# Performance work log

Measured on AMD Instinct MI355X. Metric: run time of the kernel, lower is better.

Reference implementation:

```python
import math
import jax, jax.numpy as jnp
import numpy as np


def get_alibi_slopes(n_heads: int) -> jnp.ndarray:
    def _pow2_slopes(n):
        i = jnp.arange(1, n + 1, dtype=jnp.float32)
        return jnp.power(2.0, -8.0 * i / n)
    if n_heads & (n_heads - 1) == 0:
        return _pow2_slopes(n_heads)
    nearest = 2 ** math.ceil(math.log2(n_heads))
    full = _pow2_slopes(nearest)
    half = nearest // 2
    half_slopes = _pow2_slopes(half)
    extra = full[jnp.arange(half) * 2 + 1]
    return jnp.concatenate([half_slopes, extra])[:n_heads]


def build_alibi_bias(n_heads: int, T: int, causal: bool = True) -> jnp.ndarray:
    slopes = get_alibi_slopes(n_heads)  # (H,)
    idx = jnp.arange(T)
    rel = jnp.abs(idx[:, None] - idx[None, :]).astype(jnp.float32)  # (T,T)
    bias = -slopes[:, None, None] * rel[None]  # (H,T,T)
    if causal:
        future = idx[None, :] > idx[:, None]
        bias = jnp.where(future[None], -jnp.inf, bias)
    return bias


def setup_inputs() -> dict:
    key = jax.random.key(0)
    ks = jax.random.split(key, 5)
    B, T, C = 2, 2048, 1024
    s = 0.02
    return {
        "x": jax.random.normal(ks[0], (B, T, C), dtype=jnp.float32),
        "Wq": jax.random.normal(ks[1], (C, C), dtype=jnp.float32) * s,
        "Wk": jax.random.normal(ks[2], (C, C), dtype=jnp.float32) * s,
        "Wv": jax.random.normal(ks[3], (C, C), dtype=jnp.float32) * s,
        "Wo": jax.random.normal(ks[4], (C, C), dtype=jnp.float32) * s,
    }


def reference(x, Wq, Wk, Wv, Wo):
    B, T, C = x.shape
    H = 16
    D = C // H
    scale = D ** -0.5
    # torch nn.Linear(bias=False): y = x @ W.T
    def proj_split(W):
        t = jnp.einsum('btc,dc->btd', x, W)
        return t.reshape(B, T, H, D).transpose(0, 2, 1, 3)  # (B,H,T,D)
    q, k, v = proj_split(Wq), proj_split(Wk), proj_split(Wv)
    scores = jnp.einsum('bhtd,bhsd->bhts', q, k) * scale  # (B,H,T,T)
    bias = build_alibi_bias(H, T, causal=True)  # (H,T,T)
    scores = scores + bias[None]
    attn = jax.nn.softmax(scores, axis=-1)
    out = jnp.einsum('bhts,bhsd->bhtd', attn, v)
    out = out.transpose(0, 2, 1, 3).reshape(B, T, C)
    return jnp.einsum('btc,dc->btd', out, Wo)
```

## Files before the change

### kernel.cpp

```cpp
#include <hip/hip_runtime.h>
#include <hip/hip_bf16.h>


typedef _Float16 f16;
typedef f16 f16x2 __attribute__((ext_vector_type(2)));
typedef f16 f16x4 __attribute__((ext_vector_type(4)));
typedef f16 f16x8 __attribute__((ext_vector_type(8)));
typedef float f32x4 __attribute__((ext_vector_type(4)));
typedef float f32x16 __attribute__((ext_vector_type(16)));

#define LOG2E 1.4426950408889634f
#define LDA 72
#define LDV 136

typedef const __attribute__((address_space(1))) unsigned int* gas1;
typedef __attribute__((address_space(3))) unsigned int* las3;
__device__ __forceinline__ void gload16(const f16* g, f16* l) {
  __builtin_amdgcn_global_load_lds((gas1)g, (las3)l, 16, 0, 0);
}

__device__ __forceinline__ f16x4 pk4(f32x4 v) {
  f16x2 a = __builtin_bit_cast(f16x2, __builtin_amdgcn_cvt_pkrtz(v[0], v[1]));
  f16x2 b = __builtin_bit_cast(f16x2, __builtin_amdgcn_cvt_pkrtz(v[2], v[3]));
  f16x4 r; r[0] = a[0]; r[1] = a[1]; r[2] = b[0]; r[3] = b[1];
  return r;
}
__device__ __forceinline__ f16x8 mkp(const float* e, int p) {
  f16x2 a = __builtin_bit_cast(f16x2, __builtin_amdgcn_cvt_pkrtz(e[4*p+0], e[4*p+1]));
  f16x2 b = __builtin_bit_cast(f16x2, __builtin_amdgcn_cvt_pkrtz(e[4*p+2], e[4*p+3]));
  f16x2 c = __builtin_bit_cast(f16x2, __builtin_amdgcn_cvt_pkrtz(e[8+4*p+0], e[8+4*p+1]));
  f16x2 d = __builtin_bit_cast(f16x2, __builtin_amdgcn_cvt_pkrtz(e[8+4*p+2], e[8+4*p+3]));
  f16x8 r;
  r[0]=a[0]; r[1]=a[1]; r[2]=b[0]; r[3]=b[1];
  r[4]=c[0]; r[5]=c[1]; r[6]=d[0]; r[7]=d[1];
  return r;
}

__global__ __launch_bounds__(256) void cvt_f32_f16(
    const float* __restrict__ x, const float* __restrict__ wq,
    const float* __restrict__ wk, const float* __restrict__ wv,
    const float* __restrict__ wo,
    f16* __restrict__ dx, f16* __restrict__ dwq, f16* __restrict__ dwk,
    f16* __restrict__ dwv, f16* __restrict__ dwo) {
  const float* src; f16* dst; int n;
  switch (blockIdx.y) {
    case 0:  src = x;  dst = dx;  n = 4194304; break;
    case 1:  src = wq; dst = dwq; n = 1048576; break;
    case 2:  src = wk; dst = dwk; n = 1048576; break;
    case 3:  src = wv; dst = dwv; n = 1048576; break;
    default: src = wo; dst = dwo; n = 1048576; break;
  }
  int i = (blockIdx.x * 256 + (int)threadIdx.x) * 8;
  if (i >= n) return;
  f32x4 a = *(const f32x4*)(src + i);
  f32x4 b = *(const f32x4*)(src + i + 4);
  f16x8 o;
  f16x4 lo4 = pk4(a), hi4 = pk4(b);
#pragma unroll
  for (int j = 0; j < 4; j++) { o[j] = lo4[j]; o[j + 4] = hi4[j]; }
  *(f16x8*)(dst + i) = o;
}

__device__ __forceinline__ void gemm_core(const f16* __restrict__ A,
                                          const f16* __restrict__ W,
                                          int m0, int n0,
                                          f16* lA, f16* lW,
                                          f32x4 acc[4][4]) {
  const int tid = threadIdx.x;
  const int lane = tid & 63, w = tid >> 6;
  const int wm = w & 1, wn = w >> 1;
  const int q = lane & 15, quad = lane >> 4;
  const int lrow = lane >> 2, lcol = (lane & 3) * 8;

  for (int kt = 0; kt < 1024; kt += 32) {
    __syncthreads();
#pragma unroll
    for (int t = 0; t < 2; t++) {
      const int slot = t * 4 + w;
      const int row = slot * 16 + lrow;
      gload16(A + (m0 + row) * 1024 + kt + lcol, lA + slot * 512);
      gload16(W + (n0 + row) * 1024 + kt + lcol, lW + slot * 512);
    }
    __syncthreads();
    f16x8 aF[4], bF[4];
#pragma unroll
    for (int mt = 0; mt < 4; mt++)
      aF[mt] = *(const f16x8*)(lA + (wm * 64 + mt * 16 + q) * 32 + quad * 8);
#pragma unroll
    for (int nt = 0; nt < 4; nt++)
      bF[nt] = *(const f16x8*)(lW + (wn * 64 + nt * 16 + q) * 32 + quad * 8);
#pragma unroll
    for (int mt = 0; mt < 4; mt++)
#pragma unroll
      for (int nt = 0; nt < 4; nt++)
        acc[mt][nt] = __builtin_amdgcn_mfma_f32_16x16x32_f16(aF[mt], bF[nt], acc[mt][nt], 0, 0, 0);
  }
}

__global__ __launch_bounds__(256) void qkv_proj(
    const f16* __restrict__ x16, const f16* __restrict__ wq16,
    const f16* __restrict__ wk16, const f16* __restrict__ wv16,
    f16* __restrict__ qb, f16* __restrict__ kb, f16* __restrict__ vb,
    float qscale) {
  __shared__ __align__(16) f16 lA[128 * 32];
  __shared__ __align__(16) f16 lW[128 * 32];
  const int m0 = blockIdx.x * 128, n0 = blockIdx.y * 128;
  const int z = blockIdx.z;
  const f16* W = (z == 0) ? wq16 : (z == 1) ? wk16 : wv16;
  f16* out = (z == 0) ? qb : (z == 1) ? kb : vb;
  const float scale = (z == 0) ? qscale : 1.0f;

  f32x4 acc[4][4];
  const f32x4 zero = {0.f, 0.f, 0.f, 0.f};
#pragma unroll
  for (int i = 0; i < 4; i++)
#pragma unroll
    for (int j = 0; j < 4; j++) acc[i][j] = zero;
  gemm_core(x16, W, m0, n0, lA, lW, acc);

  const int tid = threadIdx.x, lane = tid & 63, w = tid >> 6;
  const int wm = w & 1, wn = w >> 1, q = lane & 15, quad = lane >> 4;
#pragma unroll
  for (int mt = 0; mt < 4; mt++)
#pragma unroll
    for (int nt = 0; nt < 4; nt++) {
      int n = n0 + wn * 64 + nt * 16 + q;
      int h = n >> 6, d = n & 63;
#pragma unroll
      for (int r = 0; r < 4; r++) {
        int mm = m0 + wm * 64 + mt * 16 + quad * 4 + r;
        int bb = mm >> 11, tl = mm & 2047;
        out[((bb * 16 + h) * 2048 + tl) * 64 + d] = (f16)(acc[mt][nt][r] * scale);
      }
    }
}

__global__ __launch_bounds__(256) void attn(
    const f16* __restrict__ qB, const f16* __restrict__ kB,
    const f16* __restrict__ vB, f16* __restrict__ att) {
  __shared__ __align__(16) f16 lK[128 * LDA];
  __shared__ __align__(16) f16 lV[64 * LDV];
  const int tid = threadIdx.x, lane = tid & 63, w = tid >> 6;
  const int n5 = lane & 31, hh = lane >> 5;
  const int bh = blockIdx.x, qb_ = 15 - (int)blockIdx.y;
  const int b = bh >> 4, h = bh & 15;
  const int q0 = qb_ * 128;
  const f16* qP = qB + (bh * 2048) * 64;
  const f16* kP = kB + (bh * 2048) * 64;
  const f16* vP = vB + (bh * 2048) * 64;

  const float slope2 = __builtin_amdgcn_exp2f(-0.5f * (float)(h + 1)) * LOG2E;
  const int qg = q0 + w * 32 + n5;
  const int qlast = q0 + w * 32 + 31;
  const int wdiag = ((q0 + w * 32) >> 6) << 6;

  f16x8 qF[4];
#pragma unroll
  for (int ks = 0; ks < 4; ks++)
    qF[ks] = *(const f16x8*)(qP + qg * 64 + ks * 16 + hh * 8);

  f32x16 cinit, ot0, ot1;
#pragma unroll
  for (int i = 0; i < 16; i++) { cinit[i] = -8.0f; ot0[i] = 0.f; ot1[i] = 0.f; }
  float lsum = 0.0f;

  const int kr = tid >> 2, kc = (tid & 3) * 8;
  const int pp = kr & 31;
  const int mperm = (pp & 3) + 16 * ((pp >> 2) & 1) + 4 * ((pp >> 3) & 1) + 8 * ((pp >> 4) & 1);
  const int lkr = (kr & 32) + mperm;
  const int vp = (tid & 63) * 2, vd0 = (tid >> 6) * 8;

  f16x8 kA0, kA1, kB0, kB1, vA0, vA1, vB0, vB1;
  kA0 = *(const f16x8*)(kP + kr * 64 + kc);
  kA1 = *(const f16x8*)(kP + kr * 64 + kc + 32);
  kB0 = *(const f16x8*)(kP + (64 + kr) * 64 + kc);
  kB1 = *(const f16x8*)(kP + (64 + kr) * 64 + kc + 32);
  vA0 = *(const f16x8*)(vP + vp * 64 + vd0);
  vA1 = *(const f16x8*)(vP + (vp + 1) * 64 + vd0);
  vB0 = *(const f16x8*)(vP + vp * 64 + vd0 + 32);
  vB1 = *(const f16x8*)(vP + (vp + 1) * 64 + vd0 + 32);

  const int nstage = qb_ + 1;
  for (int stg = 0; stg < nstage; stg++) {
    const int kv0 = stg << 7;
    __syncthreads();
    *(f16x8*)(lK + lkr * LDA + kc) = kA0;
    *(f16x8*)(lK + lkr * LDA + kc + 32) = kA1;
    *(f16x8*)(lK + (64 + lkr) * LDA + kc) = kB0;
    *(f16x8*)(lK + (64 + lkr) * LDA + kc + 32) = kB1;
#pragma unroll
    for (int j = 0; j < 8; j++) {
      f16x2 t0; t0[0] = vA0[j]; t0[1] = vA1[j];
      *(f16x2*)(lV + (vd0 + j) * LDV + vp) = t0;
      f16x2 t1; t1[0] = vB0[j]; t1[1] = vB1[j];
      *(f16x2*)(lV + (vd0 + 32 + j) * LDV + vp) = t1;
    }
    __syncthreads();
    if (stg + 1 < nstage) {
      const int kn = kv0 + 128;
      kA0 = *(const f16x8*)(kP + (kn + kr) * 64 + kc);
      kA1 = *(const f16x8*)(kP + (kn + kr) * 64 + kc + 32);
      kB0 = *(const f16x8*)(kP + (kn + 64 + kr) * 64 + kc);
      kB1 = *(const f16x8*)(kP + (kn + 64 + kr) * 64 + kc + 32);
      vA0 = *(const f16x8*)(vP + (kn + vp) * 64 + vd0);
      vA1 = *(const f16x8*)(vP + (kn + vp + 1) * 64 + vd0);
      vB0 = *(const f16x8*)(vP + (kn + vp) * 64 + vd0 + 32);
      vB1 = *(const f16x8*)(vP + (kn + vp + 1) * 64 + vd0 + 32);
    }
#pragma unroll
    for (int half = 0; half < 2; half++) {
      const int kvh = kv0 + half * 64;
      if (kvh > wdiag) break;
      const bool act1 = (kvh + 32 <= qlast);
      const bool needmask = (kvh == wdiag);
      f32x16 s0 = cinit, s1 = cinit;
#pragma unroll
      for (int ks = 0; ks < 4; ks++) {
        f16x8 kf = *(const f16x8*)(lK + (half * 64 + n5) * LDA + ks * 16 + hh * 8);
        s0 = __builtin_amdgcn_mfma_f32_32x32x16_f16(kf, qF[ks], s0, 0, 0, 0);
      }
      if (act1) {
#pragma unroll
        for (int ks = 0; ks < 4; ks++) {
          f16x8 kf = *(const f16x8*)(lK + (half * 64 + 32 + n5) * LDA + ks * 16 + hh * 8);
          s1 = __builtin_amdgcn_mfma_f32_32x32x16_f16(kf, qF[ks], s1, 0, 0, 0);
        }
      }
      f16x8 pf00, pf01, pf10, pf11;
      {
        const int dQ = qg - kvh - 8 * hh;
        const float base0 = -slope2 * (float)dQ;
        float ev[16];
#pragma unroll
        for (int u = 0; u < 4; u++)
#pragma unroll
          for (int t = 0; t < 4; t++) {
            const int reg = t + 4 * u;
            const int CR = 16 * (u & 1) + 4 * (u >> 1) + t;
            float val = s0[reg] + fmaf(slope2, (float)CR, base0);
            if (needmask) val = (dQ >= CR) ? val : -1e30f;
            float e = __builtin_amdgcn_exp2f(val);
            lsum += e;
            ev[reg] = e;
          }
        pf00 = mkp(ev, 0); pf01 = mkp(ev, 1);
        if (act1) {
          const int dQ1 = dQ - 32;
          const float base1 = -slope2 * (float)dQ1;
          float ev1[16];
#pragma unroll
          for (int u = 0; u < 4; u++)
#pragma unroll
            for (int t = 0; t < 4; t++) {
              const int reg = t + 4 * u;
              const int CR = 16 * (u & 1) + 4 * (u >> 1) + t;
              float val = s1[reg] + fmaf(slope2, (float)CR, base1);
              if (needmask) val = (dQ1 >= CR) ? val : -1e30f;
              float e = __builtin_amdgcn_exp2f(val);
              lsum += e;
              ev1[reg] = e;
            }
          pf10 = mkp(ev1, 0); pf11 = mkp(ev1, 1);
        }
      }
#pragma unroll
      for (int p = 0; p < 2; p++) {
        f16x8 vf0 = *(const f16x8*)(lV + n5 * LDV + half * 64 + p * 16 + hh * 8);
        f16x8 vf1 = *(const f16x8*)(lV + (32 + n5) * LDV + half * 64 + p * 16 + hh * 8);
        f16x8 pf = p ? pf01 : pf00;
        ot0 = __builtin_amdgcn_mfma_f32_32x32x16_f16(vf0, pf, ot0, 0, 0, 0);
        ot1 = __builtin_amdgcn_mfma_f32_32x32x16_f16(vf1, pf, ot1, 0, 0, 0);
      }
      if (act1) {
#pragma unroll
        for (int p = 0; p < 2; p++) {
          f16x8 vf0 = *(const f16x8*)(lV + n5 * LDV + half * 64 + 32 + p * 16 + hh * 8);
          f16x8 vf1 = *(const f16x8*)(lV + (32 + n5) * LDV + half * 64 + 32 + p * 16 + hh * 8);
          f16x8 pf = p ? pf11 : pf10;
          ot0 = __builtin_amdgcn_mfma_f32_32x32x16_f16(vf0, pf, ot0, 0, 0, 0);
          ot1 = __builtin_amdgcn_mfma_f32_32x32x16_f16(vf1, pf, ot1, 0, 0, 0);
        }
      }
    }
  }

  lsum += __shfl_xor(lsum, 32);
  const float inv = 1.0f / lsum;

  __syncthreads();
  f16* OT = lK + w * (32 * LDA);
#pragma unroll
  for (int dt = 0; dt < 2; dt++)
#pragma unroll
    for (int u = 0; u < 4; u++) {
      f16x4 o4;
#pragma unroll
      for (int t = 0; t < 4; t++) {
        float v = (dt ? ot1[t + 4 * u] : ot0[t + 4 * u]) * inv;
        o4[t] = (f16)v;
      }
      *(f16x4*)(OT + n5 * LDA + dt * 32 + 8 * u + 4 * hh) = o4;
    }
  __syncthreads();
  const int row = lane >> 1, hr = lane & 1;
  const f16* OR = lK + w * (32 * LDA) + row * LDA + hr * 32;
  f16* dst = att + (b * 2048 + q0 + w * 32 + row) * 1024 + h * 64 + hr * 32;
#pragma unroll
  for (int j = 0; j < 4; j++)
    *(f16x8*)(dst + j * 8) = *(const f16x8*)(OR + j * 8);
}

__global__ __launch_bounds__(256) void out_proj(
    const f16* __restrict__ att, const f16* __restrict__ wo16,
    float* __restrict__ out) {
  __shared__ __align__(16) f16 lA[128 * 32];
  __shared__ __align__(16) f16 lW[128 * 32];
  const int m0 = blockIdx.x * 128, n0 = blockIdx.y * 128;
  f32x4 acc[4][4];
  const f32x4 zero = {0.f, 0.f, 0.f, 0.f};
#pragma unroll
  for (int i = 0; i < 4; i++)
#pragma unroll
    for (int j = 0; j < 4; j++) acc[i][j] = zero;
  gemm_core(att, wo16, m0, n0, lA, lW, acc);

  const int tid = threadIdx.x, lane = tid & 63, w = tid >> 6;
  const int wm = w & 1, wn = w >> 1, q = lane & 15, quad = lane >> 4;
#pragma unroll
  for (int mt = 0; mt < 4; mt++)
#pragma unroll
    for (int nt = 0; nt < 4; nt++) {
      int n = n0 + wn * 64 + nt * 16 + q;
#pragma unroll
      for (int r = 0; r < 4; r++) {
        int mm = m0 + wm * 64 + mt * 16 + quad * 4 + r;
        out[mm * 1024 + n] = acc[mt][nt][r];
      }
    }
}

extern "C" void kernel_launch(void* const* d_in, const int* in_sizes, int n_in,
                              void* d_out, int out_size, void* d_ws, size_t ws_size,
                              hipStream_t stream) {
  const float* x  = (const float*)d_in[0];
  const float* Wq = (const float*)d_in[1];
  const float* Wk = (const float*)d_in[2];
  const float* Wv = (const float*)d_in[3];
  const float* Wo = (const float*)d_in[4];
  char* ws = (char*)d_ws;
  const size_t MB = 1024 * 1024;
  f16* x16  = (f16*)(ws);
  f16* qb   = (f16*)(ws + 8 * MB);
  f16* kb   = (f16*)(ws + 16 * MB);
  f16* vb   = (f16*)(ws + 24 * MB);
  f16* wq16 = (f16*)(ws + 32 * MB);
  f16* wk16 = (f16*)(ws + 34 * MB);
  f16* wv16 = (f16*)(ws + 36 * MB);
  f16* wo16 = (f16*)(ws + 38 * MB);
  f16* att  = x16;

  cvt_f32_f16<<<dim3(2048, 5), 256, 0, stream>>>(x, Wq, Wk, Wv, Wo,
                                                 x16, wq16, wk16, wv16, wo16);
  qkv_proj<<<dim3(32, 8, 3), 256, 0, stream>>>(x16, wq16, wk16, wv16,
                                               qb, kb, vb, 0.125f * LOG2E);
  attn<<<dim3(32, 16), 256, 0, stream>>>(qb, kb, vb, att);
  out_proj<<<dim3(32, 8), 256, 0, stream>>>(att, wo16, (float*)d_out);
}
```

Baseline: 186.6 us.

## Split attention into 64-query blocks of two waves and tree-reduce row sums

The attention kernel now uses 128-thread blocks, each covering 64 queries instead of 128, with twice as many blocks along the query axis. This gives finer causal load balancing and more blocks per CU. The K/V staging loads were rewritten so 128 threads each load a full K row and four V rows, then transpose V into shared memory. The per-element running sum is replaced by a tree reduction to shorten the dependency chain. In exchange, each block stages the full 128-key tile for only 64 queries, so K/V traffic per query doubles, and each thread holds more registers for staging.

```diff
diff --git a/kernel.cpp b/kernel.cpp
--- a/kernel.cpp
+++ b/kernel.cpp
@@ -135,16 +135,16 @@
     }
 }
 
-__global__ __launch_bounds__(256) void attn(
+__global__ __launch_bounds__(128, 2) void attn(
     const f16* __restrict__ qB, const f16* __restrict__ kB,
     const f16* __restrict__ vB, f16* __restrict__ att) {
   __shared__ __align__(16) f16 lK[128 * LDA];
   __shared__ __align__(16) f16 lV[64 * LDV];
   const int tid = threadIdx.x, lane = tid & 63, w = tid >> 6;
   const int n5 = lane & 31, hh = lane >> 5;
-  const int bh = blockIdx.x, qb_ = 15 - (int)blockIdx.y;
+  const int bh = blockIdx.x, qi = 31 - (int)blockIdx.y;
   const int b = bh >> 4, h = bh & 15;
-  const int q0 = qb_ * 128;
+  const int q0 = qi * 64;
   const f16* qP = qB + (bh * 2048) * 64;
   const f16* kP = kB + (bh * 2048) * 64;
   const f16* vP = vB + (bh * 2048) * 64;
@@ -164,48 +164,49 @@
   for (int i = 0; i < 16; i++) { cinit[i] = -8.0f; ot0[i] = 0.f; ot1[i] = 0.f; }
   float lsum = 0.0f;
 
-  const int kr = tid >> 2, kc = (tid & 3) * 8;
+  const int kr = tid;
   const int pp = kr & 31;
   const int mperm = (pp & 3) + 16 * ((pp >> 2) & 1) + 4 * ((pp >> 3) & 1) + 8 * ((pp >> 4) & 1);
-  const int lkr = (kr & 32) + mperm;
-  const int vp = (tid & 63) * 2, vd0 = (tid >> 6) * 8;
-
-  f16x8 kA0, kA1, kB0, kB1, vA0, vA1, vB0, vB1;
-  kA0 = *(const f16x8*)(kP + kr * 64 + kc);
-  kA1 = *(const f16x8*)(kP + kr * 64 + kc + 32);
-  kB0 = *(const f16x8*)(kP + (64 + kr) * 64 + kc);
-  kB1 = *(const f16x8*)(kP + (64 + kr) * 64 + kc + 32);
-  vA0 = *(const f16x8*)(vP + vp * 64 + vd0);
-  vA1 = *(const f16x8*)(vP + (vp + 1) * 64 + vd0);
-  vB0 = *(const f16x8*)(vP + vp * 64 + vd0 + 32);
-  vB1 = *(const f16x8*)(vP + (vp + 1) * 64 + vd0 + 32);
-
-  const int nstage = qb_ + 1;
+  const int lkr = (kr & 96) + mperm;
+  const int va = (tid & 31) * 4, vd = (tid >> 5) * 16;
+
+  f16x8 kreg[8], vreg[4][2];
+#pragma unroll
+  for (int j = 0; j < 8; j++)
+    kreg[j] = *(const f16x8*)(kP + kr * 64 + j * 8);
+#pragma unroll
+  for (int r = 0; r < 4; r++) {
+    vreg[r][0] = *(const f16x8*)(vP + (va + r) * 64 + vd);
+    vreg[r][1] = *(const f16x8*)(vP + (va + r) * 64 + vd + 8);
+  }
+
+  const int nstage = (qi >> 1) + 1;
   for (int stg = 0; stg < nstage; stg++) {
     const int kv0 = stg << 7;
     __syncthreads();
-    *(f16x8*)(lK + lkr * LDA + kc) = kA0;
-    *(f16x8*)(lK + lkr * LDA + kc + 32) = kA1;
-    *(f16x8*)(lK + (64 + lkr) * LDA + kc) = kB0;
-    *(f16x8*)(lK + (64 + lkr) * LDA + kc + 32) = kB1;
-#pragma unroll
-    for (int j = 0; j < 8; j++) {
-      f16x2 t0; t0[0] = vA0[j]; t0[1] = vA1[j];
-      *(f16x2*)(lV + (vd0 + j) * LDV + vp) = t0;
-      f16x2 t1; t1[0] = vB0[j]; t1[1] = vB1[j];
-      *(f16x2*)(lV + (vd0 + 32 + j) * LDV + vp) = t1;
-    }
+#pragma unroll
+    for (int j = 0; j < 8; j++)
+      *(f16x8*)(lK + lkr * LDA + j * 8) = kreg[j];
+#pragma unroll
+    for (int s2 = 0; s2 < 2; s2++)
+#pragma unroll
+      for (int j = 0; j < 8; j++) {
+        f16x4 t;
+        t[0] = vreg[0][s2][j]; t[1] = vreg[1][s2][j];
+        t[2] = vreg[2][s2][j]; t[3] = vreg[3][s2][j];
+        *(f16x4*)(lV + (vd + s2 * 8 + j) * LDV + va) = t;
+      }
     __syncthreads();
     if (stg + 1 < nstage) {
       const int kn = kv0 + 128;
-      kA0 = *(const f16x8*)(kP + (kn + kr) * 64 + kc);
-      kA1 = *(const f16x8*)(kP + (kn + kr) * 64 + kc + 32);
-      kB0 = *(const f16x8*)(kP + (kn + 64 + kr) * 64 + kc);
-      kB1 = *(const f16x8*)(kP + (kn + 64 + kr) * 64 + kc + 32);
-      vA0 = *(const f16x8*)(vP + (kn + vp) * 64 + vd0);
-      vA1 = *(const f16x8*)(vP + (kn + vp + 1) * 64 + vd0);
-      vB0 = *(const f16x8*)(vP + (kn + vp) * 64 + vd0 + 32);
-      vB1 = *(const f16x8*)(vP + (kn + vp + 1) * 64 + vd0 + 32);
+#pragma unroll
+      for (int j = 0; j < 8; j++)
+        kreg[j] = *(const f16x8*)(kP + (kn + kr) * 64 + j * 8);
+#pragma unroll
+      for (int r = 0; r < 4; r++) {
+        vreg[r][0] = *(const f16x8*)(vP + (kn + va + r) * 64 + vd);
+        vreg[r][1] = *(const f16x8*)(vP + (kn + va + r) * 64 + vd + 8);
+      }
     }
 #pragma unroll
     for (int half = 0; half < 2; half++) {
@@ -239,10 +240,10 @@
             const int CR = 16 * (u & 1) + 4 * (u >> 1) + t;
             float val = s0[reg] + fmaf(slope2, (float)CR, base0);
             if (needmask) val = (dQ >= CR) ? val : -1e30f;
-            float e = __builtin_amdgcn_exp2f(val);
-            lsum += e;
-            ev[reg] = e;
+            ev[reg] = __builtin_amdgcn_exp2f(val);
           }
+        lsum += (((ev[0]+ev[1])+(ev[2]+ev[3])) + ((ev[4]+ev[5])+(ev[6]+ev[7])))
+              + (((ev[8]+ev[9])+(ev[10]+ev[11])) + ((ev[12]+ev[13])+(ev[14]+ev[15])));
         pf00 = mkp(ev, 0); pf01 = mkp(ev, 1);
         if (act1) {
           const int dQ1 = dQ - 32;
@@ -256,10 +257,10 @@
               const int CR = 16 * (u & 1) + 4 * (u >> 1) + t;
               float val = s1[reg] + fmaf(slope2, (float)CR, base1);
               if (needmask) val = (dQ1 >= CR) ? val : -1e30f;
-              float e = __builtin_amdgcn_exp2f(val);
-              lsum += e;
-              ev1[reg] = e;
+              ev1[reg] = __builtin_amdgcn_exp2f(val);
             }
+          lsum += (((ev1[0]+ev1[1])+(ev1[2]+ev1[3])) + ((ev1[4]+ev1[5])+(ev1[6]+ev1[7])))
+                + (((ev1[8]+ev1[9])+(ev1[10]+ev1[11])) + ((ev1[12]+ev1[13])+(ev1[14]+ev1[15])));
           pf10 = mkp(ev1, 0); pf11 = mkp(ev1, 1);
         }
       }
@@ -363,6 +364,6 @@
                                                  x16, wq16, wk16, wv16, wo16);
   qkv_proj<<<dim3(32, 8, 3), 256, 0, stream>>>(x16, wq16, wk16, wv16,
                                                qb, kb, vb, 0.125f * LOG2E);
-  attn<<<dim3(32, 16), 256, 0, stream>>>(qb, kb, vb, att);
+  attn<<<dim3(32, 32), 128, 0, stream>>>(qb, kb, vb, att);
   out_proj<<<dim3(32, 8), 256, 0, stream>>>(att, wo16, (float*)d_out);
 }
```

Result: slower. 192.1 us (+2.9%).

## Double-buffer GEMM LDS tiles with register prefetch and padded stride

Applied to the files above, without the earlier changes.

The shared GEMM core no longer uses direct global-to-LDS loads with two barriers per K step. It now prefetches the next K slice into registers while computing on the current one, writes into alternating LDS buffers, and needs only one barrier per iteration. The LDS row stride is padded from 32 to 40 halves to reduce bank conflicts on the fragment reads. The cost is more VGPRs for the prefetch registers and twice the LDS footprint per block, which could lower occupancy.

```diff
diff --git a/kernel.cpp b/kernel.cpp
--- a/kernel.cpp
+++ b/kernel.cpp
@@ -10,14 +10,9 @@
 typedef float f32x16 __attribute__((ext_vector_type(16)));
 
 #define LOG2E 1.4426950408889634f
+#define LDK 40
 #define LDA 72
 #define LDV 136
-
-typedef const __attribute__((address_space(1))) unsigned int* gas1;
-typedef __attribute__((address_space(3))) unsigned int* las3;
-__device__ __forceinline__ void gload16(const f16* g, f16* l) {
-  __builtin_amdgcn_global_load_lds((gas1)g, (las3)l, 16, 0, 0);
-}
 
 __device__ __forceinline__ f16x4 pk4(f32x4 v) {
   f16x2 a = __builtin_bit_cast(f16x2, __builtin_amdgcn_cvt_pkrtz(v[0], v[1]));
@@ -70,25 +65,39 @@
   const int lane = tid & 63, w = tid >> 6;
   const int wm = w & 1, wn = w >> 1;
   const int q = lane & 15, quad = lane >> 4;
-  const int lrow = lane >> 2, lcol = (lane & 3) * 8;
-
-  for (int kt = 0; kt < 1024; kt += 32) {
-    __syncthreads();
-#pragma unroll
-    for (int t = 0; t < 2; t++) {
-      const int slot = t * 4 + w;
-      const int row = slot * 16 + lrow;
-      gload16(A + (m0 + row) * 1024 + kt + lcol, lA + slot * 512);
-      gload16(W + (n0 + row) * 1024 + kt + lcol, lW + slot * 512);
+  const int r0 = tid >> 2, c0 = (tid & 3) * 8;
+
+  const f16* Ap = A + (m0 + r0) * 1024 + c0;
+  const f16* Wp = W + (n0 + r0) * 1024 + c0;
+  f16x8 a0 = *(const f16x8*)(Ap);
+  f16x8 a1 = *(const f16x8*)(Ap + 64 * 1024);
+  f16x8 w0 = *(const f16x8*)(Wp);
+  f16x8 w1 = *(const f16x8*)(Wp + 64 * 1024);
+
+#pragma unroll 2
+  for (int r = 0; r < 32; r++) {
+    const int p = r & 1;
+    f16* dA = lA + p * (128 * LDK);
+    f16* dW = lW + p * (128 * LDK);
+    *(f16x8*)(dA + r0 * LDK + c0) = a0;
+    *(f16x8*)(dA + (64 + r0) * LDK + c0) = a1;
+    *(f16x8*)(dW + r0 * LDK + c0) = w0;
+    *(f16x8*)(dW + (64 + r0) * LDK + c0) = w1;
+    if (r + 1 < 32) {
+      const int kn = (r + 1) * 32;
+      a0 = *(const f16x8*)(Ap + kn);
+      a1 = *(const f16x8*)(Ap + 64 * 1024 + kn);
+      w0 = *(const f16x8*)(Wp + kn);
+      w1 = *(const f16x8*)(Wp + 64 * 1024 + kn);
     }
     __syncthreads();
     f16x8 aF[4], bF[4];
 #pragma unroll
     for (int mt = 0; mt < 4; mt++)
-      aF[mt] = *(const f16x8*)(lA + (wm * 64 + mt * 16 + q) * 32 + quad * 8);
+      aF[mt] = *(const f16x8*)(dA + (wm * 64 + mt * 16 + q) * LDK + quad * 8);
 #pragma unroll
     for (int nt = 0; nt < 4; nt++)
-      bF[nt] = *(const f16x8*)(lW + (wn * 64 + nt * 16 + q) * 32 + quad * 8);
+      bF[nt] = *(const f16x8*)(dW + (wn * 64 + nt * 16 + q) * LDK + quad * 8);
 #pragma unroll
     for (int mt = 0; mt < 4; mt++)
 #pragma unroll
@@ -102,8 +111,8 @@
     const f16* __restrict__ wk16, const f16* __restrict__ wv16,
     f16* __restrict__ qb, f16* __restrict__ kb, f16* __restrict__ vb,
     float qscale) {
-  __shared__ __align__(16) f16 lA[128 * 32];
-  __shared__ __align__(16) f16 lW[128 * 32];
+  __shared__ __align__(16) f16 lA[2 * 128 * LDK];
+  __shared__ __align__(16) f16 lW[2 * 128 * LDK];
   const int m0 = blockIdx.x * 128, n0 = blockIdx.y * 128;
   const int z = blockIdx.z;
   const f16* W = (z == 0) ? wq16 : (z == 1) ? wk16 : wv16;
@@ -313,8 +322,8 @@
 __global__ __launch_bounds__(256) void out_proj(
     const f16* __restrict__ att, const f16* __restrict__ wo16,
     float* __restrict__ out) {
-  __shared__ __align__(16) f16 lA[128 * 32];
-  __shared__ __align__(16) f16 lW[128 * 32];
+  __shared__ __align__(16) f16 lA[2 * 128 * LDK];
+  __shared__ __align__(16) f16 lW[2 * 128 * LDK];
   const int m0 = blockIdx.x * 128, n0 = blockIdx.y * 128;
   f32x4 acc[4][4];
   const f32x4 zero = {0.f, 0.f, 0.f, 0.f};
```

New measurement: 186.0 us. Within noise of the previous version (-0.3%).
